# Performance work log

Hardware: AMD Instinct MI355X
Metric: run time of the kernel (lower is better)

Reference implementation:

```python
import jax, jax.numpy as jnp
import numpy as np

N_CELLS = 50000
HID = 64
DEG = 16
K_NODES = 4  # nodes per cell; cell i owns nodes [4i, 4i+4)
SP = 3


def setup_inputs() -> dict:
    key = jax.random.key(0)
    ks = jax.random.split(key, 12)
    s = 1.0 / np.sqrt(HID)
    inp = {
        'features': jax.random.normal(ks[0], (N_CELLS, HID), jnp.float32),
        'positions': jax.random.normal(ks[1], (K_NODES * N_CELLS, SP), jnp.float32),
        'neighbors': jax.random.randint(ks[2], (N_CELLS, DEG), 0, N_CELLS, jnp.int32),
        # message MLP: Linear(2H+1 -> H), SiLU, Linear(H -> H)
        'W1': jax.random.normal(ks[3], (2 * HID + 1, HID), jnp.float32) * s,
        'b1': jnp.zeros((HID,), jnp.float32),
        'W2': jax.random.normal(ks[4], (HID, HID), jnp.float32) * s,
        'b2': jnp.zeros((HID,), jnp.float32),
        # update MLP: Linear(H + H -> H), SiLU, Linear(H -> H)
        'Wu1': jax.random.normal(ks[5], (2 * HID, HID), jnp.float32) * s,
        'bu1': jnp.zeros((HID,), jnp.float32),
        'Wu2': jax.random.normal(ks[6], (HID, HID), jnp.float32) * s,
        'bu2': jnp.zeros((HID,), jnp.float32),
    }
    return inp


def reference(features, positions, neighbors, W1, b1, W2, b2, Wu1, bu1, Wu2, bu2):
    N, H = features.shape
    # centroid of each cell's owned nodes (cell i -> nodes [K*i, K*i+K))
    cent = positions.reshape(N, K_NODES, SP).mean(axis=1)          # [N, sp]
    fj = features[neighbors]                                       # [N, D, H]
    cj = cent[neighbors]                                           # [N, D, sp]
    # centroid-distance geometric invariant per (cell, neighbor) pair
    geom = jnp.linalg.norm(cent[:, None, :] - cj, axis=-1, keepdims=True)  # [N, D, 1]
    fi = jnp.broadcast_to(features[:, None, :], fj.shape)          # [N, D, H]
    x = jnp.concatenate([fi, fj, geom], axis=-1)                   # [N, D, 2H+1]
    h = jax.nn.silu(x @ W1 + b1) @ W2 + b2                         # [N, D, H]
    msg = h.mean(axis=1)                                           # mean over neighbors
    u = jnp.concatenate([features, msg], axis=-1)                  # [N, 2H]
    upd = jax.nn.silu(u @ Wu1 + bu1) @ Wu2 + bu2
    updated_features = features + upd
    return updated_features, positions
```

## Files before the change

### kernel.cpp

```cpp
#include <hip/hip_runtime.h>


#define DEG 16

typedef __attribute__((ext_vector_type(8))) short short8;
typedef __attribute__((ext_vector_type(4))) float f32x4;
typedef uint2 uint2_a __attribute__((may_alias));
typedef uint4 uint4_a __attribute__((may_alias));
typedef unsigned short ushort_a __attribute__((may_alias));

union HbRd { uint4_a u; short8 s; };
union Frag { short8 s; uint4 u; };

__device__ __forceinline__ unsigned f2bf(float f) {
  unsigned u = __float_as_uint(f);
  return (u + 0x7FFFu + ((u >> 16) & 1u)) >> 16;
}
__device__ __forceinline__ float bf2f(unsigned bits16) {
  return __uint_as_float(bits16 << 16);
}
__device__ __forceinline__ float silu(float h) {
  return h / (1.f + __expf(-h));
}
__device__ __forceinline__ float silu_fast(float h) {
  return h * __builtin_amdgcn_rcpf(1.f + __expf(-h));
}

__global__ __launch_bounds__(256) void aux_kernel(
    const float* __restrict__ pos,
    const float* __restrict__ W1, const float* __restrict__ W2,
    const float* __restrict__ Wu1, const float* __restrict__ Wu2,
    float* __restrict__ outpos, float* __restrict__ cent4,
    unsigned short* __restrict__ w1pq, unsigned short* __restrict__ w2t,
    unsigned short* __restrict__ wu1t, unsigned short* __restrict__ wu2b)
{
  int t = blockIdx.x * 256 + threadIdx.x;
  if (t < 150000) {
    ((float4*)outpos)[t] = ((const float4*)pos)[t];
  } else if (t < 174576) {
    const int r = t - 150000;
    if (r < 8192) {
      const int j = r & 7, l = (r >> 3) & 15, q = (r >> 7) & 3;
      const int f = r >> 9, kk = f & 1, mt = f >> 1;
      const int k = kk * 32 + q * 8 + j;
      const int m = mt * 16 + l;
      w1pq[r] = (unsigned short)f2bf(
          (m < 64) ? W1[k * 64 + m] : W1[(k + 64) * 64 + (m - 64)]);
    } else if (r < 12288) {
      const int s = r - 8192;
      const int j = s & 7, l = (s >> 3) & 15, q = (s >> 7) & 3;
      const int f = s >> 9, kk = f & 1, mt = f >> 1;
      const int k = kk * 32 + q * 8 + j;
      w2t[s] = (unsigned short)f2bf(W2[k * 64 + mt * 16 + l]);
    } else if (r < 20480) {
      const int s = r - 12288;
      const int j = s & 7, l = (s >> 3) & 15, q = (s >> 7) & 3;
      const int f = s >> 9, kk = f & 3, mt = f >> 2;
      const int k = kk * 32 + q * 8 + j;
      wu1t[s] = (unsigned short)f2bf(Wu1[k * 64 + mt * 16 + l]);
    } else {
      const int s = r - 20480;
      const int j = s & 7, l = (s >> 3) & 15, q = (s >> 7) & 3;
      const int f = s >> 9, kk = f & 1, nt = f >> 1;
      const int k = kk * 32 + q * 8 + j;
      wu2b[s] = (unsigned short)f2bf(Wu2[k * 64 + nt * 16 + l]);
    }
  } else if (t < 224576) {
    const int i = t - 174576;
    const float4* pp = (const float4*)(pos + 12 * i);
    const float4 a = pp[0], b = pp[1], c = pp[2];
    float4 o;
    o.x = (a.x + a.w + b.z + c.y) * 0.25f;
    o.y = (a.y + b.x + b.w + c.z) * 0.25f;
    o.z = (a.z + b.y + c.x + c.w) * 0.25f;
    o.w = 0.f;
    ((float4*)cent4)[i] = o;
  }
}

__global__ __launch_bounds__(256) void prep_kernel(
    const float* __restrict__ feat,
    const unsigned short* __restrict__ w1pq,
    unsigned short* __restrict__ featb,
    unsigned char* __restrict__ Q8)
{
  const int lane = threadIdx.x & 63;
  const int wid  = threadIdx.x >> 6;
  const int quad = lane >> 4;
  const int l15  = lane & 15;
  const int tile = blockIdx.x * 4 + wid;
  const bool act = (tile < 3125);
  const int  tt  = act ? tile : 3124;
  const int  cr  = tt * 16 + l15;

  short8 xf[2];
  #pragma unroll
  for (int kk = 0; kk < 2; ++kk) {
    const float4 f0 = *(const float4*)(feat + cr * 64 + kk * 32 + quad * 8);
    const float4 f1 = *(const float4*)(feat + cr * 64 + kk * 32 + quad * 8 + 4);
    Frag v;
    v.s[0] = (short)f2bf(f0.x); v.s[1] = (short)f2bf(f0.y);
    v.s[2] = (short)f2bf(f0.z); v.s[3] = (short)f2bf(f0.w);
    v.s[4] = (short)f2bf(f1.x); v.s[5] = (short)f2bf(f1.y);
    v.s[6] = (short)f2bf(f1.z); v.s[7] = (short)f2bf(f1.w);
    xf[kk] = v.s;
    if (act) *(uint4*)(featb + cr * 64 + kk * 32 + quad * 8) = v.u;
  }

  short8 wf[4][2];
  #pragma unroll
  for (int m = 0; m < 4; ++m)
    #pragma unroll
    for (int kk = 0; kk < 2; ++kk)
      wf[m][kk] = *(const short8*)(w1pq + ((((m + 4) * 2 + kk) * 4 + quad) << 7) + l15 * 8);

  f32x4 acc[4] = {};
  #pragma unroll
  for (int kk = 0; kk < 2; ++kk)
    #pragma unroll
    for (int m = 0; m < 4; ++m)
      acc[m] = __builtin_amdgcn_mfma_f32_16x16x32_bf16(wf[m][kk], xf[kk], acc[m], 0, 0, 0);

  if (act) {
    #pragma unroll
    for (int m = 0; m < 4; ++m) {
      int w = __builtin_amdgcn_cvt_pk_fp8_f32(acc[m][0], acc[m][1], 0, false);
      w = __builtin_amdgcn_cvt_pk_fp8_f32(acc[m][2], acc[m][3], w, true);
      *(unsigned int*)(Q8 + cr * 64 + m * 16 + quad * 4) = (unsigned)w;
    }
  }
}

__global__ __launch_bounds__(256) void msg_tail_kernel(
    const unsigned short* __restrict__ featb,
    const unsigned char* __restrict__ Q8,
    const float4* __restrict__ cent4,
    const int* __restrict__ nbr,
    const float* __restrict__ feat,
    const unsigned short* __restrict__ w1pq,
    const unsigned short* __restrict__ w2t,
    const unsigned short* __restrict__ wu1t,
    const unsigned short* __restrict__ wu2b,
    const float* __restrict__ b1, const float* __restrict__ W1,
    const float* __restrict__ b2, const float* __restrict__ bu1,
    const float* __restrict__ bu2,
    float* __restrict__ outf)
{
  __shared__ uint4 smem[432];
  char* sT  = (char*)smem;
  char* Msg = sT + 2304;
  char* Hb  = sT + 4608;

  const int lane = threadIdx.x & 63;
  const int wid  = threadIdx.x >> 6;
  const int quad = lane >> 4;
  const int l15  = lane & 15;
  const int tile = blockIdx.x;
  const int cr   = tile * 16 + l15;

  {
    short8 wpf[2];
    #pragma unroll
    for (int kk = 0; kk < 2; ++kk)
      wpf[kk] = *(const short8*)(w1pq + (((wid * 2 + kk) * 4 + quad) << 7) + l15 * 8);
    f32x4 accp = {};
    #pragma unroll
    for (int kk = 0; kk < 2; ++kk) {
      const short8 bf = *(const short8*)(featb + cr * 64 + kk * 32 + quad * 8);
      accp = __builtin_amdgcn_mfma_f32_16x16x32_bf16(wpf[kk], bf, accp, 0, 0, 0);
    }
    uint2 pk;
    pk.x = f2bf(accp[0]) | (f2bf(accp[1]) << 16);
    pk.y = f2bf(accp[2]) | (f2bf(accp[3]) << 16);
    *(uint2_a*)(sT + l15 * 144 + wid * 32 + quad * 8) = pk;
  }

  __syncthreads();

  const float b1l = b1[lane];
  const float wl  = W1[8192 + lane];

  #pragma unroll
  for (int i = 0; i < 4; ++i) {
    const int c  = tile * 16 + wid * 4 + i;
    const int cs = __builtin_amdgcn_readfirstlane(c);
    const int* nrow = nbr + cs * DEG;

    const int njl = nrow[lane & 15];
    const float4 ci = cent4[cs];
    const float4 cj = cent4[njl];
    const float dx = ci.x - cj.x, dy = ci.y - cj.y, dz = ci.z - cj.z;
    const float g = sqrtf(dx * dx + dy * dy + dz * dz);

    const float pcb =
        bf2f(((const ushort_a*)(sT + (wid * 4 + i) * 144))[lane]) + b1l;

    float acc = 0.f;
    #pragma unroll
    for (int d = 0; d < DEG; ++d) {
      const int   nd = nrow[d];
      const float gd = __uint_as_float(
          __builtin_amdgcn_readlane((int)__float_as_uint(g), d));
      const float qv = __builtin_amdgcn_cvt_f32_fp8((int)Q8[nd * 64 + lane], 0);
      acc += silu_fast(pcb + qv + gd * wl);
    }
    ((ushort_a*)(sT + (wid * 4 + i) * 144))[lane] =
        (unsigned short)f2bf(acc * 0.0625f);
  }

  short8 w2f[2], wu1f[4], wu2f[2];
  #pragma unroll
  for (int kk = 0; kk < 2; ++kk)
    w2f[kk]  = *(const short8*)(w2t  + (((wid * 2 + kk) * 4 + quad) << 7) + l15 * 8);
  #pragma unroll
  for (int kk = 0; kk < 4; ++kk)
    wu1f[kk] = *(const short8*)(wu1t + (((wid * 4 + kk) * 4 + quad) << 7) + l15 * 8);
  #pragma unroll
  for (int kk = 0; kk < 2; ++kk)
    wu2f[kk] = *(const short8*)(wu2b + (((wid * 2 + kk) * 4 + quad) << 7) + l15 * 8);

  const f32x4 b2f  = *(const f32x4*)(b2  + wid * 16 + quad * 4);
  const f32x4 bu1f = *(const f32x4*)(bu1 + wid * 16 + quad * 4);
  const float bu2v = bu2[wid * 16 + l15];

  __syncthreads();

  f32x4 accm = {};
  #pragma unroll
  for (int kk = 0; kk < 2; ++kk) {
    HbRd t; t.u = *(const uint4_a*)(sT + l15 * 144 + kk * 64 + quad * 16);
    accm = __builtin_amdgcn_mfma_f32_16x16x32_bf16(w2f[kk], t.s, accm, 0, 0, 0);
  }
  {
    uint2 pk;
    pk.x = f2bf(accm[0] + b2f[0]) | (f2bf(accm[1] + b2f[1]) << 16);
    pk.y = f2bf(accm[2] + b2f[2]) | (f2bf(accm[3] + b2f[3]) << 16);
    *(uint2_a*)(Msg + l15 * 144 + wid * 32 + quad * 8) = pk;
  }
  __syncthreads();

  f32x4 accu = {};
  #pragma unroll
  for (int kk = 0; kk < 4; ++kk) {
    short8 bf;
    if (kk < 2) {
      bf = *(const short8*)(featb + cr * 64 + kk * 32 + quad * 8);
    } else {
      HbRd t; t.u = *(const uint4_a*)(Msg + l15 * 144 + (kk - 2) * 64 + quad * 16);
      bf = t.s;
    }
    accu = __builtin_amdgcn_mfma_f32_16x16x32_bf16(wu1f[kk], bf, accu, 0, 0, 0);
  }
  {
    float sv[4];
    #pragma unroll
    for (int rg = 0; rg < 4; ++rg)
      sv[rg] = silu(accu[rg] + bu1f[rg]);
    uint2 pk;
    pk.x = f2bf(sv[0]) | (f2bf(sv[1]) << 16);
    pk.y = f2bf(sv[2]) | (f2bf(sv[3]) << 16);
    *(uint2_a*)(Hb + l15 * 144 + wid * 32 + quad * 8) = pk;
  }
  __syncthreads();

  f32x4 acc2 = {};
  #pragma unroll
  for (int kk = 0; kk < 2; ++kk) {
    HbRd t; t.u = *(const uint4_a*)(Hb + l15 * 144 + kk * 64 + quad * 16);
    acc2 = __builtin_amdgcn_mfma_f32_16x16x32_bf16(t.s, wu2f[kk], acc2, 0, 0, 0);
  }
  #pragma unroll
  for (int rg = 0; rg < 4; ++rg) {
    const int row = tile * 16 + quad * 4 + rg;
    const int col = wid * 16 + l15;
    outf[row * 64 + col] = feat[row * 64 + col] + acc2[rg] + bu2v;
  }
}

extern "C" void kernel_launch(void* const* d_in, const int* in_sizes, int n_in,
                              void* d_out, int out_size, void* d_ws, size_t ws_size,
                              hipStream_t stream)
{
  const float* feat = (const float*)d_in[0];
  const float* pos  = (const float*)d_in[1];
  const int*   nbr  = (const int*)d_in[2];
  const float* W1   = (const float*)d_in[3];
  const float* b1   = (const float*)d_in[4];
  const float* W2   = (const float*)d_in[5];
  const float* b2   = (const float*)d_in[6];
  const float* Wu1  = (const float*)d_in[7];
  const float* bu1  = (const float*)d_in[8];
  const float* Wu2  = (const float*)d_in[9];
  const float* bu2  = (const float*)d_in[10];
  float* out = (float*)d_out;

  unsigned short* featb = (unsigned short*)d_ws;
  unsigned char*  Q8    = (unsigned char*)((char*)d_ws + 12800000);
  float*          cent4 = (float*)((char*)d_ws + 25600000);
  unsigned short* w1pq  = (unsigned short*)((char*)d_ws + 26400000);
  unsigned short* w2t   = (unsigned short*)((char*)d_ws + 26416384);
  unsigned short* wu1t  = (unsigned short*)((char*)d_ws + 26424576);
  unsigned short* wu2b  = (unsigned short*)((char*)d_ws + 26440960);

  aux_kernel<<<878, 256, 0, stream>>>(pos, W1, W2, Wu1, Wu2, out + 3200000,
                                      cent4, w1pq, w2t, wu1t, wu2b);
  prep_kernel<<<782, 256, 0, stream>>>(feat, w1pq, featb, Q8);
  msg_tail_kernel<<<3125, 256, 0, stream>>>(featb, Q8, (const float4*)cent4,
                                            nbr, feat, w1pq, w2t, wu1t, wu2b,
                                            b1, W1, b2, bu1, bu2, out);
}
```

Baseline: 121.7 us.

## Merge aux and prep kernels, drop bf16 feature buffer, prefetch neighbor gathers

Folds the auxiliary kernel (position copy, weight packing, centroids) into the prep kernel as extra blocks. Prep blocks now pack their own W1 slice into shared memory, which removes the dependency on the aux output. The bf16 feature workspace is gone: the message kernel converts fp32 features itself. The message kernel also preloads neighbor indices and distances up front and double-buffers the FP8 Q8 gathers for the next cell while computing the current one. This saves one launch and the featb traffic, at the cost of more register pressure and redundant W1 packing in every prep block.

```diff
diff --git a/kernel.cpp b/kernel.cpp
--- a/kernel.cpp
+++ b/kernel.cpp
@@ -26,113 +26,135 @@
   return h * __builtin_amdgcn_rcpf(1.f + __expf(-h));
 }
 
-__global__ __launch_bounds__(256) void aux_kernel(
+__global__ __launch_bounds__(256) void prep_aux_kernel(
+    const float* __restrict__ feat,
     const float* __restrict__ pos,
     const float* __restrict__ W1, const float* __restrict__ W2,
     const float* __restrict__ Wu1, const float* __restrict__ Wu2,
     float* __restrict__ outpos, float* __restrict__ cent4,
     unsigned short* __restrict__ w1pq, unsigned short* __restrict__ w2t,
-    unsigned short* __restrict__ wu1t, unsigned short* __restrict__ wu2b)
-{
-  int t = blockIdx.x * 256 + threadIdx.x;
-  if (t < 150000) {
-    ((float4*)outpos)[t] = ((const float4*)pos)[t];
-  } else if (t < 174576) {
-    const int r = t - 150000;
-    if (r < 8192) {
-      const int j = r & 7, l = (r >> 3) & 15, q = (r >> 7) & 3;
-      const int f = r >> 9, kk = f & 1, mt = f >> 1;
-      const int k = kk * 32 + q * 8 + j;
-      const int m = mt * 16 + l;
-      w1pq[r] = (unsigned short)f2bf(
-          (m < 64) ? W1[k * 64 + m] : W1[(k + 64) * 64 + (m - 64)]);
-    } else if (r < 12288) {
-      const int s = r - 8192;
-      const int j = s & 7, l = (s >> 3) & 15, q = (s >> 7) & 3;
-      const int f = s >> 9, kk = f & 1, mt = f >> 1;
-      const int k = kk * 32 + q * 8 + j;
-      w2t[s] = (unsigned short)f2bf(W2[k * 64 + mt * 16 + l]);
-    } else if (r < 20480) {
-      const int s = r - 12288;
-      const int j = s & 7, l = (s >> 3) & 15, q = (s >> 7) & 3;
-      const int f = s >> 9, kk = f & 3, mt = f >> 2;
-      const int k = kk * 32 + q * 8 + j;
-      wu1t[s] = (unsigned short)f2bf(Wu1[k * 64 + mt * 16 + l]);
-    } else {
-      const int s = r - 20480;
-      const int j = s & 7, l = (s >> 3) & 15, q = (s >> 7) & 3;
-      const int f = s >> 9, kk = f & 1, nt = f >> 1;
-      const int k = kk * 32 + q * 8 + j;
-      wu2b[s] = (unsigned short)f2bf(Wu2[k * 64 + nt * 16 + l]);
-    }
-  } else if (t < 224576) {
-    const int i = t - 174576;
-    const float4* pp = (const float4*)(pos + 12 * i);
-    const float4 a = pp[0], b = pp[1], c = pp[2];
-    float4 o;
-    o.x = (a.x + a.w + b.z + c.y) * 0.25f;
-    o.y = (a.y + b.x + b.w + c.z) * 0.25f;
-    o.z = (a.z + b.y + c.x + c.w) * 0.25f;
-    o.w = 0.f;
-    ((float4*)cent4)[i] = o;
-  }
-}
-
-__global__ __launch_bounds__(256) void prep_kernel(
-    const float* __restrict__ feat,
-    const unsigned short* __restrict__ w1pq,
-    unsigned short* __restrict__ featb,
+    unsigned short* __restrict__ wu1t, unsigned short* __restrict__ wu2b,
     unsigned char* __restrict__ Q8)
 {
-  const int lane = threadIdx.x & 63;
-  const int wid  = threadIdx.x >> 6;
-  const int quad = lane >> 4;
-  const int l15  = lane & 15;
-  const int tile = blockIdx.x * 4 + wid;
-  const bool act = (tile < 3125);
-  const int  tt  = act ? tile : 3124;
-  const int  cr  = tt * 16 + l15;
-
-  short8 xf[2];
-  #pragma unroll
-  for (int kk = 0; kk < 2; ++kk) {
-    const float4 f0 = *(const float4*)(feat + cr * 64 + kk * 32 + quad * 8);
-    const float4 f1 = *(const float4*)(feat + cr * 64 + kk * 32 + quad * 8 + 4);
-    Frag v;
-    v.s[0] = (short)f2bf(f0.x); v.s[1] = (short)f2bf(f0.y);
-    v.s[2] = (short)f2bf(f0.z); v.s[3] = (short)f2bf(f0.w);
-    v.s[4] = (short)f2bf(f1.x); v.s[5] = (short)f2bf(f1.y);
-    v.s[6] = (short)f2bf(f1.z); v.s[7] = (short)f2bf(f1.w);
-    xf[kk] = v.s;
-    if (act) *(uint4*)(featb + cr * 64 + kk * 32 + quad * 8) = v.u;
-  }
-
-  short8 wf[4][2];
-  #pragma unroll
-  for (int m = 0; m < 4; ++m)
+  __shared__ unsigned short w1q[4096];
+
+  if (blockIdx.x < 782) {
+    const int tid  = threadIdx.x;
+    const int lane = tid & 63;
+    const int wid  = tid >> 6;
+    const int quad = lane >> 4;
+    const int l15  = lane & 15;
+
+    {
+      const int q  = (tid >> 3) & 3;
+      const int kk = (tid >> 5) & 1;
+      const int mq = tid >> 6;
+      #pragma unroll
+      for (int u = 0; u < 2; ++u) {
+        const int l = (tid * 2 + u) & 15;
+        const float* src = W1 + (64 + kk * 32 + q * 8) * 64 + mq * 16 + l;
+        unsigned short v[8];
+        #pragma unroll
+        for (int j = 0; j < 8; ++j)
+          v[j] = (unsigned short)f2bf(src[j * 64]);
+        uint4 pk;
+        pk.x = (unsigned)v[0] | ((unsigned)v[1] << 16);
+        pk.y = (unsigned)v[2] | ((unsigned)v[3] << 16);
+        pk.z = (unsigned)v[4] | ((unsigned)v[5] << 16);
+        pk.w = (unsigned)v[6] | ((unsigned)v[7] << 16);
+        ((uint4*)w1q)[tid * 2 + u] = pk;
+      }
+    }
+
+    const int tile = blockIdx.x * 4 + wid;
+    const bool act = (tile < 3125);
+    const int  tt  = act ? tile : 3124;
+    const int  cr  = tt * 16 + l15;
+
+    short8 xf[2];
+    #pragma unroll
+    for (int kk = 0; kk < 2; ++kk) {
+      const float4 f0 = *(const float4*)(feat + cr * 64 + kk * 32 + quad * 8);
+      const float4 f1 = *(const float4*)(feat + cr * 64 + kk * 32 + quad * 8 + 4);
+      Frag v;
+      v.s[0] = (short)f2bf(f0.x); v.s[1] = (short)f2bf(f0.y);
+      v.s[2] = (short)f2bf(f0.z); v.s[3] = (short)f2bf(f0.w);
+      v.s[4] = (short)f2bf(f1.x); v.s[5] = (short)f2bf(f1.y);
+      v.s[6] = (short)f2bf(f1.z); v.s[7] = (short)f2bf(f1.w);
+      xf[kk] = v.s;
+    }
+
+    __syncthreads();
+
+    short8 wf[4][2];
+    #pragma unroll
+    for (int m = 0; m < 4; ++m)
+      #pragma unroll
+      for (int kk = 0; kk < 2; ++kk)
+        wf[m][kk] = *(const short8*)(w1q + (((m * 2 + kk) * 4 + quad) << 7) + l15 * 8);
+
+    f32x4 acc[4] = {};
     #pragma unroll
     for (int kk = 0; kk < 2; ++kk)
-      wf[m][kk] = *(const short8*)(w1pq + ((((m + 4) * 2 + kk) * 4 + quad) << 7) + l15 * 8);
-
-  f32x4 acc[4] = {};
-  #pragma unroll
-  for (int kk = 0; kk < 2; ++kk)
-    #pragma unroll
-    for (int m = 0; m < 4; ++m)
-      acc[m] = __builtin_amdgcn_mfma_f32_16x16x32_bf16(wf[m][kk], xf[kk], acc[m], 0, 0, 0);
-
-  if (act) {
-    #pragma unroll
-    for (int m = 0; m < 4; ++m) {
-      int w = __builtin_amdgcn_cvt_pk_fp8_f32(acc[m][0], acc[m][1], 0, false);
-      w = __builtin_amdgcn_cvt_pk_fp8_f32(acc[m][2], acc[m][3], w, true);
-      *(unsigned int*)(Q8 + cr * 64 + m * 16 + quad * 4) = (unsigned)w;
+      #pragma unroll
+      for (int m = 0; m < 4; ++m)
+        acc[m] = __builtin_amdgcn_mfma_f32_16x16x32_bf16(wf[m][kk], xf[kk], acc[m], 0, 0, 0);
+
+    if (act) {
+      #pragma unroll
+      for (int m = 0; m < 4; ++m) {
+        int w = __builtin_amdgcn_cvt_pk_fp8_f32(acc[m][0], acc[m][1], 0, false);
+        w = __builtin_amdgcn_cvt_pk_fp8_f32(acc[m][2], acc[m][3], w, true);
+        *(unsigned int*)(Q8 + cr * 64 + m * 16 + quad * 4) = (unsigned)w;
+      }
+    }
+  } else {
+    const int t = (blockIdx.x - 782) * 256 + threadIdx.x;
+    if (t < 150000) {
+      ((float4*)outpos)[t] = ((const float4*)pos)[t];
+    } else if (t < 174576) {
+      const int r = t - 150000;
+      if (r < 8192) {
+        const int j = r & 7, l = (r >> 3) & 15, q = (r >> 7) & 3;
+        const int f = r >> 9, kk = f & 1, mt = f >> 1;
+        const int k = kk * 32 + q * 8 + j;
+        const int m = mt * 16 + l;
+        w1pq[r] = (unsigned short)f2bf(
+            (m < 64) ? W1[k * 64 + m] : W1[(k + 64) * 64 + (m - 64)]);
+      } else if (r < 12288) {
+        const int s = r - 8192;
+        const int j = s & 7, l = (s >> 3) & 15, q = (s >> 7) & 3;
+        const int f = s >> 9, kk = f & 1, mt = f >> 1;
+        const int k = kk * 32 + q * 8 + j;
+        w2t[s] = (unsigned short)f2bf(W2[k * 64 + mt * 16 + l]);
+      } else if (r < 20480) {
+        const int s = r - 12288;
+        const int j = s & 7, l = (s >> 3) & 15, q = (s >> 7) & 3;
+        const int f = s >> 9, kk = f & 3, mt = f >> 2;
+        const int k = kk * 32 + q * 8 + j;
+        wu1t[s] = (unsigned short)f2bf(Wu1[k * 64 + mt * 16 + l]);
+      } else {
+        const int s = r - 20480;
+        const int j = s & 7, l = (s >> 3) & 15, q = (s >> 7) & 3;
+        const int f = s >> 9, kk = f & 1, nt = f >> 1;
+        const int k = kk * 32 + q * 8 + j;
+        wu2b[s] = (unsigned short)f2bf(Wu2[k * 64 + nt * 16 + l]);
+      }
+    } else if (t < 224576) {
+      const int i = t - 174576;
+      const float4* pp = (const float4*)(pos + 12 * i);
+      const float4 a = pp[0], b = pp[1], c = pp[2];
+      float4 o;
+      o.x = (a.x + a.w + b.z + c.y) * 0.25f;
+      o.y = (a.y + b.x + b.w + c.z) * 0.25f;
+      o.z = (a.z + b.y + c.x + c.w) * 0.25f;
+      o.w = 0.f;
+      ((float4*)cent4)[i] = o;
     }
   }
 }
 
 __global__ __launch_bounds__(256) void msg_tail_kernel(
-    const unsigned short* __restrict__ featb,
     const unsigned char* __restrict__ Q8,
     const float4* __restrict__ cent4,
     const int* __restrict__ nbr,
@@ -158,6 +180,38 @@
   const int tile = blockIdx.x;
   const int cr   = tile * 16 + l15;
 
+  const float b1l = b1[lane];
+  const float wl  = W1[8192 + lane];
+
+  int nj[4];
+  #pragma unroll
+  for (int i = 0; i < 4; ++i) {
+    const int cs = __builtin_amdgcn_readfirstlane(tile * 16 + wid * 4 + i);
+    nj[i] = nbr[cs * DEG + l15];
+  }
+  float g[4];
+  #pragma unroll
+  for (int i = 0; i < 4; ++i) {
+    const int cs = __builtin_amdgcn_readfirstlane(tile * 16 + wid * 4 + i);
+    const float4 ci = cent4[cs];
+    const float4 cj = cent4[nj[i]];
+    const float dx = ci.x - cj.x, dy = ci.y - cj.y, dz = ci.z - cj.z;
+    g[i] = sqrtf(dx * dx + dy * dy + dz * dz);
+  }
+
+  Frag xf[2];
+  #pragma unroll
+  for (int kk = 0; kk < 2; ++kk) {
+    const float4 f0 = *(const float4*)(feat + cr * 64 + kk * 32 + quad * 8);
+    const float4 f1 = *(const float4*)(feat + cr * 64 + kk * 32 + quad * 8 + 4);
+    Frag v;
+    v.s[0] = (short)f2bf(f0.x); v.s[1] = (short)f2bf(f0.y);
+    v.s[2] = (short)f2bf(f0.z); v.s[3] = (short)f2bf(f0.w);
+    v.s[4] = (short)f2bf(f1.x); v.s[5] = (short)f2bf(f1.y);
+    v.s[6] = (short)f2bf(f1.z); v.s[7] = (short)f2bf(f1.w);
+    xf[kk] = v;
+  }
+
   {
     short8 wpf[2];
     #pragma unroll
@@ -165,43 +219,42 @@
       wpf[kk] = *(const short8*)(w1pq + (((wid * 2 + kk) * 4 + quad) << 7) + l15 * 8);
     f32x4 accp = {};
     #pragma unroll
-    for (int kk = 0; kk < 2; ++kk) {
-      const short8 bf = *(const short8*)(featb + cr * 64 + kk * 32 + quad * 8);
-      accp = __builtin_amdgcn_mfma_f32_16x16x32_bf16(wpf[kk], bf, accp, 0, 0, 0);
-    }
+    for (int kk = 0; kk < 2; ++kk)
+      accp = __builtin_amdgcn_mfma_f32_16x16x32_bf16(wpf[kk], xf[kk].s, accp, 0, 0, 0);
     uint2 pk;
     pk.x = f2bf(accp[0]) | (f2bf(accp[1]) << 16);
     pk.y = f2bf(accp[2]) | (f2bf(accp[3]) << 16);
     *(uint2_a*)(sT + l15 * 144 + wid * 32 + quad * 8) = pk;
   }
 
+  unsigned qA[16], qB[16];
+  #pragma unroll
+  for (int d = 0; d < 16; ++d) {
+    const int nd = __builtin_amdgcn_readlane(nj[0], d);
+    qA[d] = Q8[nd * 64 + lane];
+  }
+
   __syncthreads();
 
-  const float b1l = b1[lane];
-  const float wl  = W1[8192 + lane];
-
   #pragma unroll
   for (int i = 0; i < 4; ++i) {
-    const int c  = tile * 16 + wid * 4 + i;
-    const int cs = __builtin_amdgcn_readfirstlane(c);
-    const int* nrow = nbr + cs * DEG;
-
-    const int njl = nrow[lane & 15];
-    const float4 ci = cent4[cs];
-    const float4 cj = cent4[njl];
-    const float dx = ci.x - cj.x, dy = ci.y - cj.y, dz = ci.z - cj.z;
-    const float g = sqrtf(dx * dx + dy * dy + dz * dz);
-
+    unsigned (&qc)[16] = (i & 1) ? qB : qA;
+    unsigned (&qn)[16] = (i & 1) ? qA : qB;
+    if (i < 3) {
+      #pragma unroll
+      for (int d = 0; d < 16; ++d) {
+        const int nd = __builtin_amdgcn_readlane(nj[i + 1], d);
+        qn[d] = Q8[nd * 64 + lane];
+      }
+    }
     const float pcb =
         bf2f(((const ushort_a*)(sT + (wid * 4 + i) * 144))[lane]) + b1l;
-
     float acc = 0.f;
     #pragma unroll
-    for (int d = 0; d < DEG; ++d) {
-      const int   nd = nrow[d];
+    for (int d = 0; d < 16; ++d) {
       const float gd = __uint_as_float(
-          __builtin_amdgcn_readlane((int)__float_as_uint(g), d));
-      const float qv = __builtin_amdgcn_cvt_f32_fp8((int)Q8[nd * 64 + lane], 0);
+          __builtin_amdgcn_readlane((int)__float_as_uint(g[i]), d));
+      const float qv = __builtin_amdgcn_cvt_f32_fp8((int)qc[d], 0);
       acc += silu_fast(pcb + qv + gd * wl);
     }
     ((ushort_a*)(sT + (wid * 4 + i) * 144))[lane] =
@@ -244,7 +297,7 @@
   for (int kk = 0; kk < 4; ++kk) {
     short8 bf;
     if (kk < 2) {
-      bf = *(const short8*)(featb + cr * 64 + kk * 32 + quad * 8);
+      bf = xf[kk].s;
     } else {
       HbRd t; t.u = *(const uint4_a*)(Msg + l15 * 144 + (kk - 2) * 64 + quad * 16);
       bf = t.s;
@@ -294,7 +347,6 @@
   const float* bu2  = (const float*)d_in[10];
   float* out = (float*)d_out;
 
-  unsigned short* featb = (unsigned short*)d_ws;
   unsigned char*  Q8    = (unsigned char*)((char*)d_ws + 12800000);
   float*          cent4 = (float*)((char*)d_ws + 25600000);
   unsigned short* w1pq  = (unsigned short*)((char*)d_ws + 26400000);
@@ -302,10 +354,10 @@
   unsigned short* wu1t  = (unsigned short*)((char*)d_ws + 26424576);
   unsigned short* wu2b  = (unsigned short*)((char*)d_ws + 26440960);
 
-  aux_kernel<<<878, 256, 0, stream>>>(pos, W1, W2, Wu1, Wu2, out + 3200000,
-                                      cent4, w1pq, w2t, wu1t, wu2b);
-  prep_kernel<<<782, 256, 0, stream>>>(feat, w1pq, featb, Q8);
-  msg_tail_kernel<<<3125, 256, 0, stream>>>(featb, Q8, (const float4*)cent4,
-                                            nbr, feat, w1pq, w2t, wu1t, wu2b,
+  prep_aux_kernel<<<1660, 256, 0, stream>>>(feat, pos, W1, W2, Wu1, Wu2,
+                                            out + 3200000, cent4,
+                                            w1pq, w2t, wu1t, wu2b, Q8);
+  msg_tail_kernel<<<3125, 256, 0, stream>>>(Q8, (const float4*)cent4, nbr, feat,
+                                            w1pq, w2t, wu1t, wu2b,
                                             b1, W1, b2, bu1, bu2, out);
 }
```

New measurement: 118.7 us. 2.4% less time.
